# Performance work log

Hardware: AMD Instinct MI355X
Metric: run time of the kernel (lower is better)

Reference implementation:

```python
import jax, jax.numpy as jnp
import numpy as np

B, IN, OUT = 2048, 256, 256

def setup_inputs() -> dict:
    key = jax.random.key(0)
    k1, k2, k3 = jax.random.split(key, 3)
    x = jax.random.normal(k1, (B, IN), dtype=jnp.float32)
    weight = jax.random.normal(k2, (OUT, IN + 1), dtype=jnp.float32)
    w = jax.random.normal(k3, (OUT, IN + 1), dtype=jnp.float32)
    return {"x": x, "weight": weight, "w": w}

def reference(x, weight, w):
    # append bias column of ones: [B, IN+1]
    x_ext = jnp.concatenate([x, jnp.ones((x.shape[0], 1), dtype=x.dtype)], axis=1)
    # y[b,o] = sum_i weight[o,i] * sin(w[o,i] * x_ext[b,i])
    # broadcast to [B, OUT, IN+1], fused sin+mul, reduce over i
    y = jnp.sum(weight[None, :, :] * jnp.sin(w[None, :, :] * x_ext[:, None, :]), axis=2)
    return y
```

## Files before the change

### kernel.cpp

```cpp
#include <hip/hip_runtime.h>


#define IN_DIM 256
#define OUT_DIM 256
#define LDW 257
#define BTILE 8
#define OTILE 16

__global__ __launch_bounds__(256, 4)
void skan_kernel(const float* __restrict__ x,
                 const float* __restrict__ weight,
                 const float* __restrict__ wfreq,
                 float* __restrict__ y)
{
    const int tid  = threadIdx.x;
    const int lane = tid & 63;
    const int wave = tid >> 6;
    const int iq   = lane & 15;
    const int og   = wave * 4 + (lane >> 4);

    const int obase = (blockIdx.x & 15) * OTILE;
    const int b0    = (blockIdx.x >> 4) * BTILE;
    const int o     = obase + og;

    const float* wr = wfreq  + o * LDW;
    const float* gr = weight + o * LDW;

    float acc[BTILE];
#pragma unroll
    for (int b = 0; b < BTILE; ++b) acc[b] = 0.f;

#pragma unroll
    for (int c = 0; c < 4; ++c) {
        const int i = c * 64 + iq * 4;
        const float w0 = wr[i], w1 = wr[i + 1], w2 = wr[i + 2], w3 = wr[i + 3];
        const float g0 = gr[i], g1 = gr[i + 1], g2 = gr[i + 2], g3 = gr[i + 3];
#pragma unroll
        for (int b = 0; b < BTILE; ++b) {
            const float4 xv = *(const float4*)(x + (b0 + b) * IN_DIM + i);
            float a = acc[b];
            a = fmaf(g0, __sinf(w0 * xv.x), a);
            a = fmaf(g1, __sinf(w1 * xv.y), a);
            a = fmaf(g2, __sinf(w2 * xv.z), a);
            a = fmaf(g3, __sinf(w3 * xv.w), a);
            acc[b] = a;
        }
    }

    const float bias = gr[IN_DIM] * __sinf(wr[IN_DIM]);
    const float sel  = (iq == 0) ? bias : 0.f;
#pragma unroll
    for (int b = 0; b < BTILE; ++b) acc[b] += sel;

#pragma unroll
    for (int b = 0; b < BTILE; ++b) {
        float v = acc[b];
        v += __shfl_xor(v, 1);
        v += __shfl_xor(v, 2);
        v += __shfl_xor(v, 4);
        v += __shfl_xor(v, 8);
        acc[b] = v;
    }

    if (iq == 0) {
#pragma unroll
        for (int b = 0; b < BTILE; ++b) {
            y[(b0 + b) * OUT_DIM + o] = acc[b];
        }
    }
}

extern "C" void kernel_launch(void* const* d_in, const int* in_sizes, int n_in,
                              void* d_out, int out_size, void* d_ws, size_t ws_size,
                              hipStream_t stream) {
    const float* x      = (const float*)d_in[0];
    const float* weight = (const float*)d_in[1];
    const float* wfreq  = (const float*)d_in[2];
    float* y            = (float*)d_out;

    const int B = in_sizes[0] / IN_DIM;
    const int grid = (OUT_DIM / OTILE) * (B / BTILE);

    skan_kernel<<<grid, 256, 0, stream>>>(x, weight, wfreq, y);
}
```

Measured before the change: 80.96 us.

## Restructure to batch-per-lane mapping with LDS-staged x and raw hardware sine

```diff
diff --git a/kernel.cpp b/kernel.cpp
--- a/kernel.cpp
+++ b/kernel.cpp
@@ -4,8 +4,8 @@
 #define IN_DIM 256
 #define OUT_DIM 256
 #define LDW 257
-#define BTILE 8
-#define OTILE 16
+#define LXS 65
+#define INV_2PI 0.15915494309189535f
 
 __global__ __launch_bounds__(256, 4)
 void skan_kernel(const float* __restrict__ x,
@@ -13,61 +13,72 @@
                  const float* __restrict__ wfreq,
                  float* __restrict__ y)
 {
-    const int tid  = threadIdx.x;
-    const int lane = tid & 63;
-    const int wave = tid >> 6;
-    const int iq   = lane & 15;
-    const int og   = wave * 4 + (lane >> 4);
+    __shared__ float lx[64 * LXS];
 
-    const int obase = (blockIdx.x & 15) * OTILE;
-    const int b0    = (blockIdx.x >> 4) * BTILE;
-    const int o     = obase + og;
+    const int t  = threadIdx.x;
+    const int l  = t & 63;
+    const int wv = __builtin_amdgcn_readfirstlane(t >> 6);
 
-    const float* wr = wfreq  + o * LDW;
-    const float* gr = weight + o * LDW;
+    const int obase = (blockIdx.x & 31) * 8;
+    const int b0    = (blockIdx.x >> 5) * 64;
 
-    float acc[BTILE];
+    const int o0 = obase + wv * 2;
+    const int o1 = o0 + 1;
+    const float* __restrict__ w0r = wfreq  + o0 * LDW;
+    const float* __restrict__ g0r = weight + o0 * LDW;
+    const float* __restrict__ w1r = wfreq  + o1 * LDW;
+    const float* __restrict__ g1r = weight + o1 * LDW;
+
+    const int srow = wv * 16 + (l >> 4);
+    const int scol = (l & 15) * 4;
+
+    float acc0 = g0r[IN_DIM] * __builtin_amdgcn_sinf(w0r[IN_DIM] * INV_2PI);
+    float acc1 = g1r[IN_DIM] * __builtin_amdgcn_sinf(w1r[IN_DIM] * INV_2PI);
+
+    {
+        const float* gx = x + b0 * IN_DIM;
 #pragma unroll
-    for (int b = 0; b < BTILE; ++b) acc[b] = 0.f;
-
-#pragma unroll
-    for (int c = 0; c < 4; ++c) {
-        const int i = c * 64 + iq * 4;
-        const float w0 = wr[i], w1 = wr[i + 1], w2 = wr[i + 2], w3 = wr[i + 3];
-        const float g0 = gr[i], g1 = gr[i + 1], g2 = gr[i + 2], g3 = gr[i + 3];
-#pragma unroll
-        for (int b = 0; b < BTILE; ++b) {
-            const float4 xv = *(const float4*)(x + (b0 + b) * IN_DIM + i);
-            float a = acc[b];
-            a = fmaf(g0, __sinf(w0 * xv.x), a);
-            a = fmaf(g1, __sinf(w1 * xv.y), a);
-            a = fmaf(g2, __sinf(w2 * xv.z), a);
-            a = fmaf(g3, __sinf(w3 * xv.w), a);
-            acc[b] = a;
+        for (int k = 0; k < 4; ++k) {
+            const int r = srow + 4 * k;
+            const float4 v = *(const float4*)(gx + r * IN_DIM + scol);
+            float* d = &lx[r * LXS + scol];
+            d[0] = v.x * INV_2PI; d[1] = v.y * INV_2PI;
+            d[2] = v.z * INV_2PI; d[3] = v.w * INV_2PI;
         }
     }
 
-    const float bias = gr[IN_DIM] * __sinf(wr[IN_DIM]);
-    const float sel  = (iq == 0) ? bias : 0.f;
+    for (int ic = 0; ic < 4; ++ic) {
+        __syncthreads();
+
+        float xs[64];
 #pragma unroll
-    for (int b = 0; b < BTILE; ++b) acc[b] += sel;
+        for (int j = 0; j < 64; ++j) xs[j] = lx[l * LXS + j];
 
+        __syncthreads();
+
+        if (ic < 3) {
+            const float* gx = x + b0 * IN_DIM + (ic + 1) * 64;
 #pragma unroll
-    for (int b = 0; b < BTILE; ++b) {
-        float v = acc[b];
-        v += __shfl_xor(v, 1);
-        v += __shfl_xor(v, 2);
-        v += __shfl_xor(v, 4);
-        v += __shfl_xor(v, 8);
-        acc[b] = v;
+            for (int k = 0; k < 4; ++k) {
+                const int r = srow + 4 * k;
+                const float4 v = *(const float4*)(gx + r * IN_DIM + scol);
+                float* d = &lx[r * LXS + scol];
+                d[0] = v.x * INV_2PI; d[1] = v.y * INV_2PI;
+                d[2] = v.z * INV_2PI; d[3] = v.w * INV_2PI;
+            }
+        }
+
+        const int ib = ic * 64;
+#pragma unroll
+        for (int j = 0; j < 64; ++j) {
+            const float xv = xs[j];
+            acc0 = fmaf(g0r[ib + j], __builtin_amdgcn_sinf(w0r[ib + j] * xv), acc0);
+            acc1 = fmaf(g1r[ib + j], __builtin_amdgcn_sinf(w1r[ib + j] * xv), acc1);
+        }
     }
 
-    if (iq == 0) {
-#pragma unroll
-        for (int b = 0; b < BTILE; ++b) {
-            y[(b0 + b) * OUT_DIM + o] = acc[b];
-        }
-    }
+    y[(b0 + l) * OUT_DIM + o0] = acc0;
+    y[(b0 + l) * OUT_DIM + o1] = acc1;
 }
 
 extern "C" void kernel_launch(void* const* d_in, const int* in_sizes, int n_in,
@@ -79,7 +90,7 @@
     float* y            = (float*)d_out;
 
     const int B = in_sizes[0] / IN_DIM;
-    const int grid = (OUT_DIM / OTILE) * (B / BTILE);
+    const int grid = (B / 64) * (OUT_DIM / 8);
 
     skan_kernel<<<grid, 256, 0, stream>>>(x, weight, wfreq, y);
 }
```

Measured after the change: 75.63 us. -6.6%, faster.
